# Performance work log

Measured on AMD Instinct MI355X. Metric: run time of the kernel, lower is better.

The kernel has to match this reference:

```python
import jax, jax.numpy as jnp
import numpy as np

D_IN = 2048
D_SAE = 16384
N_RANGES = 4
CTX = 128  # batch == context_length
CHUNK = D_SAE // N_RANGES
LN_EPS = 1e-5


def setup_inputs() -> dict:
    key = jax.random.key(0)
    k1, k2, k3, k4 = jax.random.split(key, 4)
    acts = jax.random.normal(k1, (CTX, D_IN), dtype=jnp.float32)
    # orthogonal-init stand-ins: unit-variance columns
    W_enc_ranges = jax.random.normal(k2, (N_RANGES, D_IN, CHUNK), dtype=jnp.float32) / np.sqrt(D_IN)
    W_dec = jax.random.normal(k3, (D_SAE, D_IN), dtype=jnp.float32) / np.sqrt(D_SAE)
    pos_embeddings = jax.random.normal(k4, (N_RANGES, D_IN), dtype=jnp.float32) * 0.02
    return {
        "acts": acts,
        "W_enc_ranges": W_enc_ranges,
        "b_enc": jnp.zeros((D_SAE,), jnp.float32),
        "b_dec": jnp.zeros((D_IN,), jnp.float32),
        "pos_embeddings": pos_embeddings,
        "ln_weight": jnp.ones((D_SAE,), jnp.float32),
        "ln_bias": jnp.zeros((D_SAE,), jnp.float32),
        "W_dec": W_dec,
    }


def reference(acts, W_enc_ranges, b_enc, b_dec, pos_embeddings, ln_weight, ln_bias, W_dec):
    B, d_in = acts.shape
    n_ranges, _, chunk = W_enc_ranges.shape
    range_size = B // n_ranges  # positions are contiguous blocks per range
    d_sae = n_ranges * chunk

    # gather per position range: [n_ranges, range_size, d_in]
    x = acts.reshape(n_ranges, range_size, d_in)
    x = x + pos_embeddings[:, None, :] - b_dec  # (input + pos_emb) - b_dec

    # per-range GEMM + bias
    pre = jnp.einsum("rbd,rds->rbs", x, W_enc_ranges) + b_enc.reshape(n_ranges, 1, chunk)

    # per-range LayerNorm over the chunk (sliced gamma/beta), biased variance
    mu = jnp.mean(pre, axis=-1, keepdims=True)
    var = jnp.mean(jnp.square(pre - mu), axis=-1, keepdims=True)
    normed = (pre - mu) * jax.lax.rsqrt(var + LN_EPS)
    normed = normed * ln_weight.reshape(n_ranges, 1, chunk) + ln_bias.reshape(n_ranges, 1, chunk)
    feat = jax.nn.relu(normed)  # [n_ranges, range_size, chunk]

    # scatter into block-diagonal encoded [B, d_sae]
    encoded = jnp.zeros((B, d_sae), acts.dtype)
    for r in range(n_ranges):
        encoded = encoded.at[r * range_size:(r + 1) * range_size,
                             r * chunk:(r + 1) * chunk].set(feat[r])

    # decode
    decoded = encoded @ W_dec + b_dec
    return decoded
```

## Files before the change

### kernel.cpp

```cpp
#include <hip/hip_runtime.h>
#include <hip/hip_bf16.h>
#include <stdint.h>


#define D_IN   2048
#define CHUNK  4096
#define RS     32
#define LN_EPS 1e-5f

typedef __attribute__((ext_vector_type(8))) short bf16x8;
typedef __attribute__((ext_vector_type(4))) float f32x4;

#define AS1 __attribute__((address_space(1)))
#define AS3 __attribute__((address_space(3)))

__device__ __forceinline__ void gload_lds16(const float* g, float* l) {
  __builtin_amdgcn_global_load_lds((const AS1 unsigned int*)g,
                                   (AS3 unsigned int*)l, 16, 0, 0);
}

__device__ __forceinline__ unsigned short f2bf(float f) {
  unsigned int u = __float_as_uint(f);
  u += 0x7fffu + ((u >> 16) & 1u);
  return (unsigned short)(u >> 16);
}

#define MFMA16 __builtin_amdgcn_mfma_f32_16x16x32_bf16

__global__ __launch_bounds__(256) void prep_kernel(
    const float* __restrict__ acts, const float* __restrict__ pos,
    const float* __restrict__ bdec, unsigned short* __restrict__ xfrag) {
  unsigned tid = blockIdx.x * 256u + threadIdx.x;
  unsigned lane = tid & 63u, kt = (tid >> 6) & 63u, mt = (tid >> 12) & 1u, r = tid >> 13;
  unsigned m  = mt * 16 + (lane & 15u);
  unsigned k0 = kt * 32 + (lane >> 4) * 8;
  const float* ap = acts + (size_t)(r * RS + m) * D_IN + k0;
  const float* pp = pos  + (size_t)r * D_IN + k0;
  const float* bp = bdec + k0;
  bf16x8 v;
#pragma unroll
  for (int j = 0; j < 8; ++j) v[j] = (short)f2bf(ap[j] + pp[j] - bp[j]);
  *reinterpret_cast<bf16x8*>(xfrag + (size_t)tid * 8) = v;
}

__global__ __launch_bounds__(256) void enc_kernel(
    const unsigned short* __restrict__ xfrag, const float* __restrict__ Wenc,
    float* __restrict__ pre_part) {
  const unsigned r = blockIdx.x >> 8, h = (blockIdx.x >> 7) & 1u, nt = blockIdx.x & 127u;
  const unsigned n0 = nt * 32;
  const unsigned w = threadIdx.x >> 6, lane = threadIdx.x & 63u;
  const unsigned col = lane & 15u, g = lane >> 4;

  __shared__ float smem[8192];
  float* mytile = smem + w * 2048;

  const unsigned srow = lane >> 3, scol = (lane & 7u) * 4u;
  const float* gbase = Wenc
      + ((size_t)(r * D_IN + h * 1024 + w * 32 + srow)) * CHUNK + n0 + scol;
  const unsigned short* xa0 = xfrag + ((size_t)(r * 2 + 0) * 64) * 512 + (size_t)lane * 8;
  const unsigned short* xa1 = xfrag + ((size_t)(r * 2 + 1) * 64) * 512 + (size_t)lane * 8;

  f32x4 acc00 = {0.f,0.f,0.f,0.f}, acc01 = acc00, acc10 = acc00, acc11 = acc00;

  auto stageW = [&](unsigned s, unsigned b) {
#pragma unroll
    for (int l = 0; l < 4; ++l) {
      const float* gp = gbase + (size_t)(s * 128 + l * 8) * CHUNK;
      gload_lds16(gp, mytile + b * 1024 + l * 256);
    }
  };

  bf16x8 aC0, aC1, aN0, aN1;
  {
    unsigned kt = h * 32 + w;
    aC0 = *(const bf16x8*)(xa0 + (size_t)kt * 512);
    aC1 = *(const bf16x8*)(xa1 + (size_t)kt * 512);
  }
  stageW(0, 0);

  unsigned buf = 0;
#pragma unroll
  for (int s = 0; s < 8; ++s) {
    if (s < 7) {
      unsigned kt = h * 32 + (s + 1) * 4 + w;
      aN0 = *(const bf16x8*)(xa0 + (size_t)kt * 512);
      aN1 = *(const bf16x8*)(xa1 + (size_t)kt * 512);
      stageW(s + 1, buf ^ 1);
      asm volatile("s_waitcnt vmcnt(6)" ::: "memory");
    } else {
      asm volatile("s_waitcnt vmcnt(0)" ::: "memory");
    }
    const float* tb = mytile + buf * 1024 + g * 8 * 32 + col;
    bf16x8 b0, b1;
#pragma unroll
    for (int j = 0; j < 8; ++j) {
      b0[j] = (short)f2bf(tb[j * 32]);
      b1[j] = (short)f2bf(tb[j * 32 + 16]);
    }
    acc00 = MFMA16(aC0, b0, acc00, 0, 0, 0);
    acc01 = MFMA16(aC0, b1, acc01, 0, 0, 0);
    acc10 = MFMA16(aC1, b0, acc10, 0, 0, 0);
    acc11 = MFMA16(aC1, b1, acc11, 0, 0, 0);
    aC0 = aN0; aC1 = aN1; buf ^= 1;
  }

  __syncthreads();
  float* red = smem;
  if (w > 0) {
#pragma unroll
    for (int i = 0; i < 4; ++i) {
      red[(((w - 1) * 4 + 0) * 64 + lane) * 4 + i] = acc00[i];
      red[(((w - 1) * 4 + 1) * 64 + lane) * 4 + i] = acc01[i];
      red[(((w - 1) * 4 + 2) * 64 + lane) * 4 + i] = acc10[i];
      red[(((w - 1) * 4 + 3) * 64 + lane) * 4 + i] = acc11[i];
    }
  }
  __syncthreads();
  if (w == 0) {
    for (int q = 0; q < 3; ++q)
#pragma unroll
      for (int i = 0; i < 4; ++i) {
        acc00[i] += red[((q * 4 + 0) * 64 + lane) * 4 + i];
        acc01[i] += red[((q * 4 + 1) * 64 + lane) * 4 + i];
        acc10[i] += red[((q * 4 + 2) * 64 + lane) * 4 + i];
        acc11[i] += red[((q * 4 + 3) * 64 + lane) * 4 + i];
      }
    float* pp = pre_part + (size_t)h * 128 * CHUNK;
#pragma unroll
    for (int i = 0; i < 4; ++i) {
      unsigned row0 = r * RS + g * 4 + i;
      unsigned row1 = row0 + 16;
      pp[(size_t)row0 * CHUNK + n0 + col]      = acc00[i];
      pp[(size_t)row0 * CHUNK + n0 + 16 + col] = acc01[i];
      pp[(size_t)row1 * CHUNK + n0 + col]      = acc10[i];
      pp[(size_t)row1 * CHUNK + n0 + 16 + col] = acc11[i];
    }
  }
}

__global__ __launch_bounds__(256) void lnpack_kernel(
    const float* __restrict__ pre_part, const float* __restrict__ benc,
    const float* __restrict__ gamma, const float* __restrict__ beta,
    unsigned short* __restrict__ featfrag) {
  const unsigned row = blockIdx.x;
  const unsigned r = row >> 5, m = row & 31u;
  const unsigned t = threadIdx.x;
  const unsigned c0 = t * 16;

  const float* p0 = pre_part + (size_t)row * CHUNK + c0;
  const float* p1 = p0 + (size_t)128 * CHUNK;
  const float* bb = benc + (size_t)r * CHUNK + c0;

  float v[16];
  float s = 0.f, q = 0.f;
#pragma unroll
  for (int j = 0; j < 16; ++j) {
    v[j] = p0[j] + p1[j] + bb[j];
    s += v[j]; q += v[j] * v[j];
  }
#pragma unroll
  for (int off = 1; off < 64; off <<= 1) {
    s += __shfl_xor(s, off, 64);
    q += __shfl_xor(q, off, 64);
  }
  __shared__ float ls[4], lq[4];
  if ((t & 63u) == 0) { ls[t >> 6] = s; lq[t >> 6] = q; }
  __syncthreads();
  s = ls[0] + ls[1] + ls[2] + ls[3];
  q = lq[0] + lq[1] + lq[2] + lq[3];
  float mu  = s * (1.f / CHUNK);
  float var = q * (1.f / CHUNK) - mu * mu;
  float rsd = rsqrtf(var + LN_EPS);

  const float* gp = gamma + (size_t)r * CHUNK + c0;
  const float* bp = beta  + (size_t)r * CHUNK + c0;
  const unsigned mt = m >> 4;
#pragma unroll
  for (int half = 0; half < 2; ++half) {
    bf16x8 o;
#pragma unroll
    for (int j = 0; j < 8; ++j) {
      float x = (v[half * 8 + j] - mu) * rsd * gp[half * 8 + j] + bp[half * 8 + j];
      o[j] = (short)f2bf(fmaxf(x, 0.f));
    }
    unsigned k = c0 + half * 8;
    unsigned kt = k >> 5, grp = (k >> 3) & 3u, ln = (m & 15u) + 16u * grp;
    *(bf16x8*)(featfrag + (((size_t)(r * 2 + mt) * 128 + kt) * 64 + ln) * 8) = o;
  }
}

__global__ __launch_bounds__(256) void dec_kernel(
    const unsigned short* __restrict__ featfrag, const float* __restrict__ Wdec,
    float* __restrict__ part) {
  const unsigned r = blockIdx.x >> 8, h = (blockIdx.x >> 6) & 3u, nt = blockIdx.x & 63u;
  const unsigned n0 = nt * 32;
  const unsigned w = threadIdx.x >> 6, lane = threadIdx.x & 63u;
  const unsigned col = lane & 15u, g = lane >> 4;

  __shared__ float smem[8192];
  float* mytile = smem + w * 2048;

  const unsigned srow = lane >> 3, scol = (lane & 7u) * 4u;
  const float* gbase = Wdec
      + ((size_t)(r * CHUNK + h * 1024 + w * 32 + srow)) * D_IN + n0 + scol;
  const unsigned short* fa0 = featfrag + ((size_t)(r * 2 + 0) * 128) * 512 + (size_t)lane * 8;
  const unsigned short* fa1 = featfrag + ((size_t)(r * 2 + 1) * 128) * 512 + (size_t)lane * 8;

  f32x4 acc00 = {0.f,0.f,0.f,0.f}, acc01 = acc00, acc10 = acc00, acc11 = acc00;

  auto stageW = [&](unsigned s, unsigned b) {
#pragma unroll
    for (int l = 0; l < 4; ++l) {
      const float* gp = gbase + (size_t)(s * 128 + l * 8) * D_IN;
      gload_lds16(gp, mytile + b * 1024 + l * 256);
    }
  };

  bf16x8 aC0, aC1, aN0, aN1;
  {
    unsigned kt = h * 32 + w;
    aC0 = *(const bf16x8*)(fa0 + (size_t)kt * 512);
    aC1 = *(const bf16x8*)(fa1 + (size_t)kt * 512);
  }
  stageW(0, 0);

  unsigned buf = 0;
#pragma unroll
  for (int s = 0; s < 8; ++s) {
    if (s < 7) {
      unsigned kt = h * 32 + (s + 1) * 4 + w;
      aN0 = *(const bf16x8*)(fa0 + (size_t)kt * 512);
      aN1 = *(const bf16x8*)(fa1 + (size_t)kt * 512);
      stageW(s + 1, buf ^ 1);
      asm volatile("s_waitcnt vmcnt(6)" ::: "memory");
    } else {
      asm volatile("s_waitcnt vmcnt(0)" ::: "memory");
    }
    const float* tb = mytile + buf * 1024 + g * 8 * 32 + col;
    bf16x8 b0, b1;
#pragma unroll
    for (int j = 0; j < 8; ++j) {
      b0[j] = (short)f2bf(tb[j * 32]);
      b1[j] = (short)f2bf(tb[j * 32 + 16]);
    }
    acc00 = MFMA16(aC0, b0, acc00, 0, 0, 0);
    acc01 = MFMA16(aC0, b1, acc01, 0, 0, 0);
    acc10 = MFMA16(aC1, b0, acc10, 0, 0, 0);
    acc11 = MFMA16(aC1, b1, acc11, 0, 0, 0);
    aC0 = aN0; aC1 = aN1; buf ^= 1;
  }

  __syncthreads();
  float* red = smem;
  if (w > 0) {
#pragma unroll
    for (int i = 0; i < 4; ++i) {
      red[(((w - 1) * 4 + 0) * 64 + lane) * 4 + i] = acc00[i];
      red[(((w - 1) * 4 + 1) * 64 + lane) * 4 + i] = acc01[i];
      red[(((w - 1) * 4 + 2) * 64 + lane) * 4 + i] = acc10[i];
      red[(((w - 1) * 4 + 3) * 64 + lane) * 4 + i] = acc11[i];
    }
  }
  __syncthreads();
  if (w == 0) {
    for (int q = 0; q < 3; ++q)
#pragma unroll
      for (int i = 0; i < 4; ++i) {
        acc00[i] += red[((q * 4 + 0) * 64 + lane) * 4 + i];
        acc01[i] += red[((q * 4 + 1) * 64 + lane) * 4 + i];
        acc10[i] += red[((q * 4 + 2) * 64 + lane) * 4 + i];
        acc11[i] += red[((q * 4 + 3) * 64 + lane) * 4 + i];
      }
    float* pp = part + (size_t)h * 128 * D_IN;
#pragma unroll
    for (int i = 0; i < 4; ++i) {
      unsigned row0 = r * RS + g * 4 + i;
      unsigned row1 = row0 + 16;
      pp[(size_t)row0 * D_IN + n0 + col]      = acc00[i];
      pp[(size_t)row0 * D_IN + n0 + 16 + col] = acc01[i];
      pp[(size_t)row1 * D_IN + n0 + col]      = acc10[i];
      pp[(size_t)row1 * D_IN + n0 + 16 + col] = acc11[i];
    }
  }
}

__global__ __launch_bounds__(256) void finish_kernel(
    const float* __restrict__ part, const float* __restrict__ bdec,
    float* __restrict__ out) {
  unsigned i = blockIdx.x * 256u + threadIdx.x;
  const size_t stride = (size_t)128 * D_IN / 4;
  f32x4 a0 = ((const f32x4*)part)[i];
  f32x4 a1 = ((const f32x4*)part)[i + stride];
  f32x4 a2 = ((const f32x4*)part)[i + 2 * stride];
  f32x4 a3 = ((const f32x4*)part)[i + 3 * stride];
  f32x4 c  = ((const f32x4*)bdec)[i & 511u];
  f32x4 o;
#pragma unroll
  for (int j = 0; j < 4; ++j) o[j] = a0[j] + a1[j] + a2[j] + a3[j] + c[j];
  ((f32x4*)out)[i] = o;
}

extern "C" void kernel_launch(void* const* d_in, const int* in_sizes, int n_in,
                              void* d_out, int out_size, void* d_ws, size_t ws_size,
                              hipStream_t stream) {
  const float* acts = (const float*)d_in[0];
  const float* Wenc = (const float*)d_in[1];
  const float* benc = (const float*)d_in[2];
  const float* bdec = (const float*)d_in[3];
  const float* pos  = (const float*)d_in[4];
  const float* lnw  = (const float*)d_in[5];
  const float* lnb  = (const float*)d_in[6];
  const float* Wdec = (const float*)d_in[7];
  float* out = (float*)d_out;

  char* ws = (char*)d_ws;
  unsigned short* xfrag   = (unsigned short*)ws;
  float* pre_part         = (float*)(ws + 512 * 1024);
  unsigned short* featfrg = (unsigned short*)(ws + 512 * 1024 + 4 * 1024 * 1024);
  float* part             = (float*)(ws + 512 * 1024 + 5 * 1024 * 1024);

  prep_kernel  <<<128,  256, 0, stream>>>(acts, pos, bdec, xfrag);
  enc_kernel   <<<1024, 256, 0, stream>>>(xfrag, Wenc, pre_part);
  lnpack_kernel<<<128,  256, 0, stream>>>(pre_part, benc, lnw, lnb, featfrg);
  dec_kernel   <<<1024, 256, 0, stream>>>(featfrg, Wdec, part);
  finish_kernel<<<256,  256, 0, stream>>>(part, bdec, out);
}
```

Measured before the change: 66.67 us.

## Fuse split-K decode reduction via atomic last-block and store encoder partials as bf16

Removes the separate finish kernel. Each decode block now bumps an atomic counter per output tile, and the last of the four split-K blocks sums the partials, adds b_dec and writes the output. The counters are zeroed in prep_kernel. The encoder's split-K partial sums are also stored as bf16 rather than fp32, which halves that intermediate traffic. The cost is some precision in the LayerNorm inputs, plus atomic and fence overhead in the decode kernel.

```diff
diff --git a/kernel.cpp b/kernel.cpp
--- a/kernel.cpp
+++ b/kernel.cpp
@@ -24,13 +24,18 @@
   u += 0x7fffu + ((u >> 16) & 1u);
   return (unsigned short)(u >> 16);
 }
+__device__ __forceinline__ float bf2f(unsigned short s) {
+  return __uint_as_float(((unsigned int)s) << 16);
+}
 
 #define MFMA16 __builtin_amdgcn_mfma_f32_16x16x32_bf16
 
 __global__ __launch_bounds__(256) void prep_kernel(
     const float* __restrict__ acts, const float* __restrict__ pos,
-    const float* __restrict__ bdec, unsigned short* __restrict__ xfrag) {
+    const float* __restrict__ bdec, unsigned short* __restrict__ xfrag,
+    int* __restrict__ cnt) {
   unsigned tid = blockIdx.x * 256u + threadIdx.x;
+  if (blockIdx.x == 0) cnt[threadIdx.x] = 0;
   unsigned lane = tid & 63u, kt = (tid >> 6) & 63u, mt = (tid >> 12) & 1u, r = tid >> 13;
   unsigned m  = mt * 16 + (lane & 15u);
   unsigned k0 = kt * 32 + (lane >> 4) * 8;
@@ -45,7 +50,7 @@
 
 __global__ __launch_bounds__(256) void enc_kernel(
     const unsigned short* __restrict__ xfrag, const float* __restrict__ Wenc,
-    float* __restrict__ pre_part) {
+    unsigned short* __restrict__ pre_part) {
   const unsigned r = blockIdx.x >> 8, h = (blockIdx.x >> 7) & 1u, nt = blockIdx.x & 127u;
   const unsigned n0 = nt * 32;
   const unsigned w = threadIdx.x >> 6, lane = threadIdx.x & 63u;
@@ -125,21 +130,21 @@
         acc10[i] += red[((q * 4 + 2) * 64 + lane) * 4 + i];
         acc11[i] += red[((q * 4 + 3) * 64 + lane) * 4 + i];
       }
-    float* pp = pre_part + (size_t)h * 128 * CHUNK;
+    unsigned short* pp = pre_part + (size_t)h * 128 * CHUNK;
 #pragma unroll
     for (int i = 0; i < 4; ++i) {
       unsigned row0 = r * RS + g * 4 + i;
       unsigned row1 = row0 + 16;
-      pp[(size_t)row0 * CHUNK + n0 + col]      = acc00[i];
-      pp[(size_t)row0 * CHUNK + n0 + 16 + col] = acc01[i];
-      pp[(size_t)row1 * CHUNK + n0 + col]      = acc10[i];
-      pp[(size_t)row1 * CHUNK + n0 + 16 + col] = acc11[i];
+      pp[(size_t)row0 * CHUNK + n0 + col]      = f2bf(acc00[i]);
+      pp[(size_t)row0 * CHUNK + n0 + 16 + col] = f2bf(acc01[i]);
+      pp[(size_t)row1 * CHUNK + n0 + col]      = f2bf(acc10[i]);
+      pp[(size_t)row1 * CHUNK + n0 + 16 + col] = f2bf(acc11[i]);
     }
   }
 }
 
 __global__ __launch_bounds__(256) void lnpack_kernel(
-    const float* __restrict__ pre_part, const float* __restrict__ benc,
+    const unsigned short* __restrict__ pre_part, const float* __restrict__ benc,
     const float* __restrict__ gamma, const float* __restrict__ beta,
     unsigned short* __restrict__ featfrag) {
   const unsigned row = blockIdx.x;
@@ -147,17 +152,22 @@
   const unsigned t = threadIdx.x;
   const unsigned c0 = t * 16;
 
-  const float* p0 = pre_part + (size_t)row * CHUNK + c0;
-  const float* p1 = p0 + (size_t)128 * CHUNK;
+  const unsigned short* p0 = pre_part + (size_t)row * CHUNK + c0;
+  const unsigned short* p1 = p0 + (size_t)128 * CHUNK;
   const float* bb = benc + (size_t)r * CHUNK + c0;
+
+  bf16x8 u0a = *(const bf16x8*)p0, u0b = *(const bf16x8*)(p0 + 8);
+  bf16x8 u1a = *(const bf16x8*)p1, u1b = *(const bf16x8*)(p1 + 8);
 
   float v[16];
   float s = 0.f, q = 0.f;
 #pragma unroll
-  for (int j = 0; j < 16; ++j) {
-    v[j] = p0[j] + p1[j] + bb[j];
-    s += v[j]; q += v[j] * v[j];
-  }
+  for (int j = 0; j < 8; ++j) {
+    v[j]     = bf2f((unsigned short)u0a[j]) + bf2f((unsigned short)u1a[j]) + bb[j];
+    v[j + 8] = bf2f((unsigned short)u0b[j]) + bf2f((unsigned short)u1b[j]) + bb[j + 8];
+  }
+#pragma unroll
+  for (int j = 0; j < 16; ++j) { s += v[j]; q += v[j] * v[j]; }
 #pragma unroll
   for (int off = 1; off < 64; off <<= 1) {
     s += __shfl_xor(s, off, 64);
@@ -191,13 +201,15 @@
 
 __global__ __launch_bounds__(256) void dec_kernel(
     const unsigned short* __restrict__ featfrag, const float* __restrict__ Wdec,
-    float* __restrict__ part) {
+    const float* __restrict__ bdec, float* __restrict__ part,
+    int* __restrict__ cnt, float* __restrict__ out) {
   const unsigned r = blockIdx.x >> 8, h = (blockIdx.x >> 6) & 3u, nt = blockIdx.x & 63u;
   const unsigned n0 = nt * 32;
   const unsigned w = threadIdx.x >> 6, lane = threadIdx.x & 63u;
   const unsigned col = lane & 15u, g = lane >> 4;
 
   __shared__ float smem[8192];
+  __shared__ int lastflag;
   float* mytile = smem + w * 2048;
 
   const unsigned srow = lane >> 3, scol = (lane & 7u) * 4u;
@@ -281,23 +293,30 @@
       pp[(size_t)row1 * D_IN + n0 + col]      = acc10[i];
       pp[(size_t)row1 * D_IN + n0 + 16 + col] = acc11[i];
     }
-  }
-}
-
-__global__ __launch_bounds__(256) void finish_kernel(
-    const float* __restrict__ part, const float* __restrict__ bdec,
-    float* __restrict__ out) {
-  unsigned i = blockIdx.x * 256u + threadIdx.x;
-  const size_t stride = (size_t)128 * D_IN / 4;
-  f32x4 a0 = ((const f32x4*)part)[i];
-  f32x4 a1 = ((const f32x4*)part)[i + stride];
-  f32x4 a2 = ((const f32x4*)part)[i + 2 * stride];
-  f32x4 a3 = ((const f32x4*)part)[i + 3 * stride];
-  f32x4 c  = ((const f32x4*)bdec)[i & 511u];
-  f32x4 o;
-#pragma unroll
-  for (int j = 0; j < 4; ++j) o[j] = a0[j] + a1[j] + a2[j] + a3[j] + c[j];
-  ((f32x4*)out)[i] = o;
+    __threadfence();
+  }
+  __syncthreads();
+  if (threadIdx.x == 0) {
+    int old = __hip_atomic_fetch_add(&cnt[r * 64 + nt], 1,
+                                     __ATOMIC_ACQ_REL, __HIP_MEMORY_SCOPE_AGENT);
+    lastflag = (old == 3);
+  }
+  __syncthreads();
+  if (lastflag) {
+    __threadfence();
+    const unsigned rl = threadIdx.x >> 3;
+    const unsigned c  = n0 + (threadIdx.x & 7u) * 4u;
+    const size_t off = (size_t)(r * RS + rl) * D_IN + c;
+    f32x4 s0 = *(const f32x4*)(part + off);
+    f32x4 s1 = *(const f32x4*)(part + (size_t)1 * 128 * D_IN + off);
+    f32x4 s2 = *(const f32x4*)(part + (size_t)2 * 128 * D_IN + off);
+    f32x4 s3 = *(const f32x4*)(part + (size_t)3 * 128 * D_IN + off);
+    f32x4 bd = *(const f32x4*)(bdec + c);
+    f32x4 o;
+#pragma unroll
+    for (int j = 0; j < 4; ++j) o[j] = ((s0[j] + s1[j]) + (s2[j] + s3[j])) + bd[j];
+    *(f32x4*)(out + off) = o;
+  }
 }
 
 extern "C" void kernel_launch(void* const* d_in, const int* in_sizes, int n_in,
@@ -315,13 +334,13 @@
 
   char* ws = (char*)d_ws;
   unsigned short* xfrag   = (unsigned short*)ws;
-  float* pre_part         = (float*)(ws + 512 * 1024);
-  unsigned short* featfrg = (unsigned short*)(ws + 512 * 1024 + 4 * 1024 * 1024);
-  float* part             = (float*)(ws + 512 * 1024 + 5 * 1024 * 1024);
-
-  prep_kernel  <<<128,  256, 0, stream>>>(acts, pos, bdec, xfrag);
-  enc_kernel   <<<1024, 256, 0, stream>>>(xfrag, Wenc, pre_part);
-  lnpack_kernel<<<128,  256, 0, stream>>>(pre_part, benc, lnw, lnb, featfrg);
-  dec_kernel   <<<1024, 256, 0, stream>>>(featfrg, Wdec, part);
-  finish_kernel<<<256,  256, 0, stream>>>(part, bdec, out);
-}
+  unsigned short* pre_prt = (unsigned short*)(ws + 512 * 1024);
+  unsigned short* featfrg = (unsigned short*)(ws + 2560 * 1024);
+  float* part             = (float*)(ws + 3584 * 1024);
+  int* cnt                = (int*)(ws + 7680 * 1024);
+
+  prep_kernel  <<<128,  256, 0, stream>>>(acts, pos, bdec, xfrag, cnt);
+  enc_kernel   <<<1024, 256, 0, stream>>>(xfrag, Wenc, pre_prt);
+  lnpack_kernel<<<128,  256, 0, stream>>>(pre_prt, benc, lnw, lnb, featfrg);
+  dec_kernel   <<<1024, 256, 0, stream>>>(featfrg, Wdec, bdec, part, cnt, out);
+}
```

Result: slower. 172.6 us (+158.9%).
